# Performance work log

Measured on AMD Instinct MI355X. Metric: run time of the kernel, lower is better.

The kernel has to match this reference:

```python
import jax, jax.numpy as jnp
import numpy as np

B, T, V, E, H, D = 32, 64, 32000, 512, 1024, 1024
BOS, EOS, PAD, TAU = 1, 3, 0, 1.0


def setup_inputs() -> dict:
    key = jax.random.key(0)
    ks = jax.random.split(key, 8)
    s = lambda k, shape, sc=0.02: jax.random.normal(k, shape, jnp.float32) * sc
    return {
        'image_hidden': jax.random.normal(ks[0], (B, D), jnp.float32),
        'gumbel_u': jax.random.uniform(ks[1], (T, B, V), jnp.float32),
        'W_proj': s(ks[2], (H, D)), 'b_proj': jnp.zeros((H,), jnp.float32),
        'emb': s(ks[3], (V, E)),
        'W_ih': s(ks[4], (4 * H, E)), 'W_hh': s(ks[5], (4 * H, H)),
        'b_ih': jnp.zeros((4 * H,), jnp.float32), 'b_hh': jnp.zeros((4 * H,), jnp.float32),
        'W_hv': s(ks[6], (V, H)), 'b_hv': jnp.zeros((V,), jnp.float32),
    }


def lstm_cell(x, h, c, W_ih, W_hh, b_ih, b_hh):
    gates = x @ W_ih.T + h @ W_hh.T + (b_ih + b_hh)
    i, f, g, o = jnp.split(gates, 4, axis=-1)  # torch LSTM gate order
    c = jax.nn.sigmoid(f) * c + jax.nn.sigmoid(i) * jnp.tanh(g)
    h = jax.nn.sigmoid(o) * jnp.tanh(c)
    return h, c


def reference(image_hidden, gumbel_u, W_proj, b_proj, emb, W_ih, W_hh, b_ih, b_hh, W_hv, b_hv):
    # initial state from projected image representation
    h0 = image_hidden @ W_proj.T + b_proj            # [B, H]
    c0 = jnp.zeros_like(h0)
    x0 = jnp.broadcast_to(emb[BOS], (B, E))          # BOS embedding
    h, c = lstm_cell(x0, h0, c0, W_ih, W_hh, b_ih, b_hh)

    def step(carry, u):
        h, c = carry
        logit = h @ W_hv.T + b_hv                    # [B, V]
        g = -jnp.log(-jnp.log(u + 1e-10) + 1e-10)    # gumbel noise from uniform
        y_soft = jax.nn.softmax((logit + g) / TAU, axis=-1)
        label = jnp.argmax(y_soft, axis=-1)          # [B]
        y_hard = jax.nn.one_hot(label, V, dtype=y_soft.dtype)
        y = y_hard + y_soft - jax.lax.stop_gradient(y_soft)  # straight-through (hard=True)
        x = y @ emb                                  # soft embedding lookup [B, E]
        h, c = lstm_cell(x, h, c, W_ih, W_hh, b_ih, b_hh)
        return (h, c), (y, label)

    _, (ys, labels) = jax.lax.scan(step, (h, c), gumbel_u)
    logits = jnp.swapaxes(ys, 0, 1)                  # [B, T, V]
    labels = labels.T                                # [B, T]

    # force final token to EOS
    logits = logits.at[:, -1, :].set(jax.nn.one_hot(EOS, V, dtype=logits.dtype))
    labels = labels.at[:, -1].set(EOS)

    pad_g = jnp.cumsum((labels == EOS).astype(jnp.int32), axis=1) == 0  # True before first EOS
    message_ids = jnp.where(pad_g, labels, 0)
    pad_oh = jax.nn.one_hot(PAD, V, dtype=logits.dtype)
    message_logits = jnp.where(pad_g[:, :, None], logits, pad_oh)
    message_lengths = jnp.max(jnp.cumsum(pad_g.astype(jnp.int32), axis=1), axis=1) + 1
    return message_ids, message_logits, message_lengths
```

## Files before the change

kernel.cpp:

```cpp
#include <hip/hip_runtime.h>
#include <cstdint>
#include <cstddef>

#define NB 32
#define NT 64
#define NV 32000
#define NE 512
#define NH 1024
#define BOS_ID 1
#define EOS_ID 3

__device__ __forceinline__ unsigned mono_f32(float f) {
    unsigned u = __float_as_uint(f);
    return (u & 0x80000000u) ? ~u : (u | 0x80000000u);
}

__global__ __launch_bounds__(256) void k_init(const float* __restrict__ img,
                                              const float* __restrict__ Wp,
                                              const float* __restrict__ bp,
                                              float* __restrict__ h0,
                                              float* __restrict__ c) {
    int g = blockIdx.x * 256 + threadIdx.x;
    int j = g >> 5, b = g & 31;
    const float* ir = img + (size_t)b * NH;
    const float* wr = Wp + (size_t)j * NH;
    float s = bp[j];
    for (int k = 0; k < NH; k++) s = fmaf(ir[k], wr[k], s);
    h0[b * NH + j] = s;
    c[b * NH + j]  = 0.0f;
}

__global__ __launch_bounds__(256) void k_logit(const float* __restrict__ h,
                                               const float* __restrict__ Whv,
                                               const float* __restrict__ bhv,
                                               const float* __restrict__ gu,
                                               int s,
                                               unsigned long long* __restrict__ partials) {
    __shared__ float hs[32][36];
    __shared__ float wsh[32][132];
    __shared__ float red_s[32][32];
    __shared__ int   red_i[32][32];
    const int tid = threadIdx.x;
    const int blk = blockIdx.x;
    const int v0  = blk * 128;
    const int bq  = tid >> 5;
    const int vq  = tid & 31;
    float acc[4][4];
#pragma unroll
    for (int i = 0; i < 4; i++)
#pragma unroll
        for (int j = 0; j < 4; j++) acc[i][j] = 0.f;

    for (int kc = 0; kc < NH; kc += 32) {
        __syncthreads();
#pragma unroll
        for (int i = 0; i < 4; i++) {
            int idx = i * 256 + tid;
            int b = idx >> 5, kk = idx & 31;
            hs[kk][b] = h[b * NH + kc + kk];
        }
#pragma unroll
        for (int i = 0; i < 16; i++) {
            int idx = i * 256 + tid;
            int vv = idx >> 5, kk = idx & 31;
            wsh[kk][vv] = Whv[(size_t)(v0 + vv) * NH + kc + kk];
        }
        __syncthreads();
#pragma unroll
        for (int kk = 0; kk < 32; kk++) {
            float4 hv4 = *(const float4*)&hs[kk][bq * 4];
            float4 wv4 = *(const float4*)&wsh[kk][vq * 4];
            float hv[4] = {hv4.x, hv4.y, hv4.z, hv4.w};
            float wv[4] = {wv4.x, wv4.y, wv4.z, wv4.w};
#pragma unroll
            for (int bi = 0; bi < 4; bi++)
#pragma unroll
                for (int vi = 0; vi < 4; vi++)
                    acc[bi][vi] = fmaf(hv[bi], wv[vi], acc[bi][vi]);
        }
    }

    const float4 bv4 = *(const float4*)&bhv[v0 + vq * 4];
    float bvv[4] = {bv4.x, bv4.y, bv4.z, bv4.w};
#pragma unroll
    for (int bi = 0; bi < 4; bi++) {
        int b = bq * 4 + bi;
        const float4 uv4 = *(const float4*)&gu[((size_t)s * NB + b) * NV + v0 + vq * 4];
        float uvv[4] = {uv4.x, uv4.y, uv4.z, uv4.w};
        float best = -3.4e38f;
        int bidx = v0 + vq * 4;
#pragma unroll
        for (int vi = 0; vi < 4; vi++) {
            float g  = -logf(-logf(uvv[vi] + 1e-10f) + 1e-10f);
            float sc = acc[bi][vi] + bvv[vi] + g;
            if (sc > best) { best = sc; bidx = v0 + vq * 4 + vi; }
        }
        red_s[b][vq] = best;
        red_i[b][vq] = bidx;
    }
    __syncthreads();
    if (tid < 32) {
        int b = tid;
        float bs = red_s[b][0];
        int   bi = red_i[b][0];
        for (int q = 1; q < 32; q++) {
            float v = red_s[b][q];
            if (v > bs) { bs = v; bi = red_i[b][q]; }
        }
        unsigned long long key =
            ((unsigned long long)mono_f32(bs) << 32) | (unsigned)(~(unsigned)bi);
        partials[blk * 32 + b] = key;
    }
}

__global__ __launch_bounds__(256) void k_lstm(const float* __restrict__ h,
                                              float* __restrict__ hn,
                                              float* __restrict__ cbuf,
                                              const float* __restrict__ emb,
                                              const float* __restrict__ Wih,
                                              const float* __restrict__ Whh,
                                              const float* __restrict__ bih,
                                              const float* __restrict__ bhh,
                                              const unsigned long long* __restrict__ partials,
                                              int* __restrict__ hist,
                                              int s, int skip) {
    __shared__ float Wt[512][20];
    __shared__ float xh[32][517];
    __shared__ int labels[32];
    const int tid = threadIdx.x, blk = blockIdx.x;
    const int b8 = tid >> 3, ks = tid & 7;

    if (s < 0) {
        if (tid < 32) labels[tid] = BOS_ID;
    } else {
        unsigned long long best = 0ull;
        for (int p = ks; p < 250; p += 8) {
            unsigned long long k = partials[p * 32 + b8];
            if (k > best) best = k;
        }
#pragma unroll
        for (int m = 1; m < 8; m <<= 1) {
            unsigned long long o = (unsigned long long)__shfl_xor((long long)best, m, 64);
            if (o > best) best = o;
        }
        if (ks == 0) labels[b8] = (int)(~(unsigned)best);
    }
    __syncthreads();
    if (s >= 0 && blk == 0 && tid < 32) hist[s * 32 + tid] = labels[tid];
    if (skip) return;

    const int j0 = blk * 4;
    float acc[16];
#pragma unroll
    for (int r = 0; r < 16; r++) acc[r] = 0.f;

    for (int chunk = 0; chunk < 3; chunk++) {
        __syncthreads();
#pragma unroll
        for (int i = 0; i < 32; i++) {
            int idx = i * 256 + tid;
            int slot = idx >> 9, k = idx & 511;
            int gate = slot >> 2, jj = slot & 3;
            int row = gate * NH + j0 + jj;
            float w = (chunk == 0) ? Wih[(size_t)row * NE + k]
                                   : Whh[(size_t)row * NH + (chunk - 1) * 512 + k];
            Wt[k][slot] = w;
        }
#pragma unroll
        for (int i = 0; i < 64; i++) {
            int idx = i * 256 + tid;
            int b = idx >> 9, k = idx & 511;
            float xv = (chunk == 0) ? emb[(size_t)labels[b] * NE + k]
                                    : h[b * NH + (chunk - 1) * 512 + k];
            xh[b][k] = xv;
        }
        __syncthreads();
#pragma unroll 4
        for (int i = 0; i < 64; i++) {
            int k = ks + 8 * i;
            float xv = xh[b8][k];
            const float4 w0 = *(const float4*)&Wt[k][0];
            const float4 w1 = *(const float4*)&Wt[k][4];
            const float4 w2 = *(const float4*)&Wt[k][8];
            const float4 w3 = *(const float4*)&Wt[k][12];
            acc[0]  = fmaf(xv, w0.x, acc[0]);  acc[1]  = fmaf(xv, w0.y, acc[1]);
            acc[2]  = fmaf(xv, w0.z, acc[2]);  acc[3]  = fmaf(xv, w0.w, acc[3]);
            acc[4]  = fmaf(xv, w1.x, acc[4]);  acc[5]  = fmaf(xv, w1.y, acc[5]);
            acc[6]  = fmaf(xv, w1.z, acc[6]);  acc[7]  = fmaf(xv, w1.w, acc[7]);
            acc[8]  = fmaf(xv, w2.x, acc[8]);  acc[9]  = fmaf(xv, w2.y, acc[9]);
            acc[10] = fmaf(xv, w2.z, acc[10]); acc[11] = fmaf(xv, w2.w, acc[11]);
            acc[12] = fmaf(xv, w3.x, acc[12]); acc[13] = fmaf(xv, w3.y, acc[13]);
            acc[14] = fmaf(xv, w3.z, acc[14]); acc[15] = fmaf(xv, w3.w, acc[15]);
        }
    }
#pragma unroll
    for (int m = 1; m < 8; m <<= 1)
#pragma unroll
        for (int r = 0; r < 16; r++) acc[r] += __shfl_xor(acc[r], m, 64);

    if (ks == 0) {
        int b = b8;
#pragma unroll
        for (int jj = 0; jj < 4; jj++) {
            int j = j0 + jj;
            float gi = acc[0 + jj]  + bih[j]          + bhh[j];
            float gf = acc[4 + jj]  + bih[NH + j]     + bhh[NH + j];
            float gg = acc[8 + jj]  + bih[2 * NH + j] + bhh[2 * NH + j];
            float go = acc[12 + jj] + bih[3 * NH + j] + bhh[3 * NH + j];
            float si = 1.f / (1.f + expf(-gi));
            float sf = 1.f / (1.f + expf(-gf));
            float so = 1.f / (1.f + expf(-go));
            float cn = sf * cbuf[b * NH + j] + si * tanhf(gg);
            float hv = so * tanhf(cn);
            cbuf[b * NH + j] = cn;
            hn[b * NH + j]   = hv;
        }
    }
}

__global__ __launch_bounds__(64) void k_out(const int* __restrict__ hist,
                                            float* __restrict__ out) {
    int b = threadIdx.x;
    if (b >= 32) return;
    int te = 63;
    for (int t = 0; t < 63; t++)
        if (hist[t * 32 + b] == EOS_ID) { te = t; break; }
    for (int t = 0; t < 64; t++) {
        int lab = (t < 63) ? hist[t * 32 + b] : EOS_ID;
        int id = (t < te) ? lab : 0;
        out[b * 64 + t] = (float)id;
    }
    out[2048 + (size_t)NB * NT * NV + b] = (float)(te + 1);
}

__global__ __launch_bounds__(256) void k_scatter(float* __restrict__ out) {
    const int bt = blockIdx.x;
    float* row = out + 2048 + (size_t)bt * NV;
    const int id = (int)out[bt];
    float4 z = make_float4(0.f, 0.f, 0.f, 0.f);
    for (int i = threadIdx.x; i < NV / 4; i += 256) ((float4*)row)[i] = z;
    __syncthreads();
    if (threadIdx.x == 0) row[id] = 1.0f;
}

extern "C" void kernel_launch(void* const* d_in, const int* in_sizes, int n_in,
                              void* d_out, int out_size, void* d_ws, size_t ws_size,
                              hipStream_t stream) {
    const float* img = (const float*)d_in[0];
    const float* gu  = (const float*)d_in[1];
    const float* Wp  = (const float*)d_in[2];
    const float* bp  = (const float*)d_in[3];
    const float* emb = (const float*)d_in[4];
    const float* Wih = (const float*)d_in[5];
    const float* Whh = (const float*)d_in[6];
    const float* bih = (const float*)d_in[7];
    const float* bhh = (const float*)d_in[8];
    const float* Whv = (const float*)d_in[9];
    const float* bhv = (const float*)d_in[10];
    float* out = (float*)d_out;

    float* scratch = out + 2048;
    float* hA = scratch;
    float* hB = scratch + 32768;
    float* cb = scratch + 65536;
    unsigned long long* partials = (unsigned long long*)(scratch + 98304);
    int* hist = (int*)(scratch + 98304 + 16000);

    k_init<<<128, 256, 0, stream>>>(img, Wp, bp, hB, cb);
    k_lstm<<<256, 256, 0, stream>>>(hB, hA, cb, emb, Wih, Whh, bih, bhh,
                                    (const unsigned long long*)nullptr, hist, -1, 0);
    for (int s = 0; s < 63; s++) {
        const float* hc = (s & 1) ? hB : hA;
        float* hn       = (s & 1) ? hA : hB;
        k_logit<<<250, 256, 0, stream>>>(hc, Whv, bhv, gu, s, partials);
        k_lstm<<<256, 256, 0, stream>>>(hc, hn, cb, emb, Wih, Whh, bih, bhh,
                                        partials, hist, s, (s == 62) ? 1 : 0);
    }
    k_out<<<1, 64, 0, stream>>>(hist, out);
    k_scatter<<<2048, 256, 0, stream>>>(out);
}
```

Baseline: 12.64 ms.

## Double-buffer logit GEMM tiles and reduce argmax via wave shuffles plus atomicMax

The vocab-projection kernel now uses 512 threads with a 2x4 register tile and a 64-wide K chunk. Shared-memory tiles are double-buffered and the next chunk is prefetched into registers while the current one is computed. The per-block argmax runs as a wave-level shuffle reduction and combines across blocks with a 64-bit atomicMax into a ping-pong slot, so the LSTM kernel no longer scans 250 partials per row. The LSTM kernel zeros the next slot for the following step, which relies on stream ordering between kernels and adds atomic contention on 32 addresses.

After: 12.43 ms. About the same (-1.6%).

```diff
diff --git a/kernel.cpp b/kernel.cpp
--- a/kernel.cpp
+++ b/kernel.cpp
@@ -9,6 +9,7 @@
 #define NH 1024
 #define BOS_ID 1
 #define EOS_ID 3
+#define KC 64
 
 __device__ __forceinline__ unsigned mono_f32(float f) {
     unsigned u = __float_as_uint(f);
@@ -30,86 +31,110 @@
     c[b * NH + j]  = 0.0f;
 }
 
-__global__ __launch_bounds__(256) void k_logit(const float* __restrict__ h,
+__global__ __launch_bounds__(512) void k_logit(const float* __restrict__ h,
                                                const float* __restrict__ Whv,
                                                const float* __restrict__ bhv,
                                                const float* __restrict__ gu,
                                                int s,
-                                               unsigned long long* __restrict__ partials) {
-    __shared__ float hs[32][36];
-    __shared__ float wsh[32][132];
-    __shared__ float red_s[32][32];
-    __shared__ int   red_i[32][32];
+                                               unsigned long long* __restrict__ slot) {
+    __shared__ float wsh[2][KC][132];
+    __shared__ float hs[2][KC][34];
     const int tid = threadIdx.x;
-    const int blk = blockIdx.x;
-    const int v0  = blk * 128;
+    const int v0  = blockIdx.x * 128;
+    const int vq  = tid & 31;
     const int bq  = tid >> 5;
-    const int vq  = tid & 31;
-    float acc[4][4];
-#pragma unroll
-    for (int i = 0; i < 4; i++)
-#pragma unroll
-        for (int j = 0; j < 4; j++) acc[i][j] = 0.f;
-
-    for (int kc = 0; kc < NH; kc += 32) {
+    const int wq  = tid & 15;
+    const int wv  = tid >> 4;
+
+    float4 wr[4];
+    float4 hr;
+    float acc[2][4];
+#pragma unroll
+    for (int bi = 0; bi < 2; bi++)
+#pragma unroll
+        for (int j = 0; j < 4; j++) acc[bi][j] = 0.f;
+
+    auto load_chunk = [&](int kc) {
+#pragma unroll
+        for (int i = 0; i < 4; i++) {
+            int vv = i * 32 + wv;
+            wr[i] = *(const float4*)&Whv[(size_t)(v0 + vv) * NH + kc + wq * 4];
+        }
+        hr = *(const float4*)&h[wv * NH + kc + wq * 4];
+    };
+    auto store_chunk = [&](int p) {
+#pragma unroll
+        for (int i = 0; i < 4; i++) {
+            int vv = i * 32 + wv;
+            wsh[p][wq * 4 + 0][vv] = wr[i].x;
+            wsh[p][wq * 4 + 1][vv] = wr[i].y;
+            wsh[p][wq * 4 + 2][vv] = wr[i].z;
+            wsh[p][wq * 4 + 3][vv] = wr[i].w;
+        }
+        hs[p][wq * 4 + 0][wv] = hr.x;
+        hs[p][wq * 4 + 1][wv] = hr.y;
+        hs[p][wq * 4 + 2][wv] = hr.z;
+        hs[p][wq * 4 + 3][wv] = hr.w;
+    };
+
+    load_chunk(0);
+    store_chunk(0);
+    load_chunk(KC);
+
+    const int NCH = NH / KC;
+    for (int c = 0; c < NCH; c++) {
         __syncthreads();
-#pragma unroll
-        for (int i = 0; i < 4; i++) {
-            int idx = i * 256 + tid;
-            int b = idx >> 5, kk = idx & 31;
-            hs[kk][b] = h[b * NH + kc + kk];
-        }
-#pragma unroll
-        for (int i = 0; i < 16; i++) {
-            int idx = i * 256 + tid;
-            int vv = idx >> 5, kk = idx & 31;
-            wsh[kk][vv] = Whv[(size_t)(v0 + vv) * NH + kc + kk];
-        }
-        __syncthreads();
-#pragma unroll
-        for (int kk = 0; kk < 32; kk++) {
-            float4 hv4 = *(const float4*)&hs[kk][bq * 4];
-            float4 wv4 = *(const float4*)&wsh[kk][vq * 4];
-            float hv[4] = {hv4.x, hv4.y, hv4.z, hv4.w};
-            float wv[4] = {wv4.x, wv4.y, wv4.z, wv4.w};
-#pragma unroll
-            for (int bi = 0; bi < 4; bi++)
-#pragma unroll
-                for (int vi = 0; vi < 4; vi++)
-                    acc[bi][vi] = fmaf(hv[bi], wv[vi], acc[bi][vi]);
+        const int p = c & 1;
+#pragma unroll 16
+        for (int kk = 0; kk < KC; kk++) {
+            float4 wv4 = *(const float4*)&wsh[p][kk][vq * 4];
+            float2 hv2 = *(const float2*)&hs[p][kk][bq * 2];
+            acc[0][0] = fmaf(hv2.x, wv4.x, acc[0][0]);
+            acc[0][1] = fmaf(hv2.x, wv4.y, acc[0][1]);
+            acc[0][2] = fmaf(hv2.x, wv4.z, acc[0][2]);
+            acc[0][3] = fmaf(hv2.x, wv4.w, acc[0][3]);
+            acc[1][0] = fmaf(hv2.y, wv4.x, acc[1][0]);
+            acc[1][1] = fmaf(hv2.y, wv4.y, acc[1][1]);
+            acc[1][2] = fmaf(hv2.y, wv4.z, acc[1][2]);
+            acc[1][3] = fmaf(hv2.y, wv4.w, acc[1][3]);
+        }
+        if (c + 1 < NCH) {
+            store_chunk(1 - p);
+            if (c + 2 < NCH) load_chunk((c + 2) * KC);
         }
     }
 
     const float4 bv4 = *(const float4*)&bhv[v0 + vq * 4];
     float bvv[4] = {bv4.x, bv4.y, bv4.z, bv4.w};
-#pragma unroll
-    for (int bi = 0; bi < 4; bi++) {
-        int b = bq * 4 + bi;
-        const float4 uv4 = *(const float4*)&gu[((size_t)s * NB + b) * NV + v0 + vq * 4];
-        float uvv[4] = {uv4.x, uv4.y, uv4.z, uv4.w};
+    unsigned long long key[2];
+#pragma unroll
+    for (int bi = 0; bi < 2; bi++) {
+        int b = bq * 2 + bi;
+        const float4 u4 = *(const float4*)&gu[((size_t)s * NB + b) * NV + v0 + vq * 4];
+        float uvv[4] = {u4.x, u4.y, u4.z, u4.w};
         float best = -3.4e38f;
         int bidx = v0 + vq * 4;
 #pragma unroll
-        for (int vi = 0; vi < 4; vi++) {
-            float g  = -logf(-logf(uvv[vi] + 1e-10f) + 1e-10f);
-            float sc = acc[bi][vi] + bvv[vi] + g;
-            if (sc > best) { best = sc; bidx = v0 + vq * 4 + vi; }
-        }
-        red_s[b][vq] = best;
-        red_i[b][vq] = bidx;
-    }
-    __syncthreads();
-    if (tid < 32) {
-        int b = tid;
-        float bs = red_s[b][0];
-        int   bi = red_i[b][0];
-        for (int q = 1; q < 32; q++) {
-            float v = red_s[b][q];
-            if (v > bs) { bs = v; bi = red_i[b][q]; }
-        }
-        unsigned long long key =
-            ((unsigned long long)mono_f32(bs) << 32) | (unsigned)(~(unsigned)bi);
-        partials[blk * 32 + b] = key;
+        for (int j = 0; j < 4; j++) {
+            float g  = -logf(-logf(uvv[j] + 1e-10f) + 1e-10f);
+            float sc = acc[bi][j] + bvv[j] + g;
+            if (sc > best) { best = sc; bidx = v0 + vq * 4 + j; }
+        }
+        key[bi] = ((unsigned long long)mono_f32(best) << 32) | (unsigned)(~(unsigned)bidx);
+    }
+#pragma unroll
+    for (int m = 1; m < 32; m <<= 1) {
+#pragma unroll
+        for (int bi = 0; bi < 2; bi++) {
+            unsigned long long o =
+                (unsigned long long)__shfl_xor((long long)key[bi], m, 32);
+            if (o > key[bi]) key[bi] = o;
+        }
+    }
+    if (vq == 0) {
+#pragma unroll
+        for (int bi = 0; bi < 2; bi++)
+            atomicMax(&slot[(s & 1) * 32 + bq * 2 + bi], key[bi]);
     }
 }
 
@@ -121,7 +146,7 @@
                                               const float* __restrict__ Whh,
                                               const float* __restrict__ bih,
                                               const float* __restrict__ bhh,
-                                              const unsigned long long* __restrict__ partials,
+                                              unsigned long long* __restrict__ slot,
                                               int* __restrict__ hist,
                                               int s, int skip) {
     __shared__ float Wt[512][20];
@@ -133,19 +158,10 @@
     if (s < 0) {
         if (tid < 32) labels[tid] = BOS_ID;
     } else {
-        unsigned long long best = 0ull;
-        for (int p = ks; p < 250; p += 8) {
-            unsigned long long k = partials[p * 32 + b8];
-            if (k > best) best = k;
-        }
-#pragma unroll
-        for (int m = 1; m < 8; m <<= 1) {
-            unsigned long long o = (unsigned long long)__shfl_xor((long long)best, m, 64);
-            if (o > best) best = o;
-        }
-        if (ks == 0) labels[b8] = (int)(~(unsigned)best);
-    }
-    __syncthreads();
+        if (tid < 32) labels[tid] = (int)(~(unsigned)slot[(s & 1) * 32 + tid]);
+    }
+    if (tid >= 32 && tid < 64)
+        slot[((s + 1) & 1) * 32 + (tid - 32)] = 0ull;
     if (s >= 0 && blk == 0 && tid < 32) hist[s * 32 + tid] = labels[tid];
     if (skip) return;
 
@@ -159,12 +175,12 @@
 #pragma unroll
         for (int i = 0; i < 32; i++) {
             int idx = i * 256 + tid;
-            int slot = idx >> 9, k = idx & 511;
-            int gate = slot >> 2, jj = slot & 3;
+            int slot_i = idx >> 9, k = idx & 511;
+            int gate = slot_i >> 2, jj = slot_i & 3;
             int row = gate * NH + j0 + jj;
             float w = (chunk == 0) ? Wih[(size_t)row * NE + k]
                                    : Whh[(size_t)row * NH + (chunk - 1) * 512 + k];
-            Wt[k][slot] = w;
+            Wt[k][slot_i] = w;
         }
 #pragma unroll
         for (int i = 0; i < 64; i++) {
@@ -263,18 +279,18 @@
     float* hA = scratch;
     float* hB = scratch + 32768;
     float* cb = scratch + 65536;
-    unsigned long long* partials = (unsigned long long*)(scratch + 98304);
-    int* hist = (int*)(scratch + 98304 + 16000);
+    unsigned long long* slot = (unsigned long long*)(scratch + 98304);
+    int* hist = (int*)(scratch + 98304 + 128);
 
     k_init<<<128, 256, 0, stream>>>(img, Wp, bp, hB, cb);
     k_lstm<<<256, 256, 0, stream>>>(hB, hA, cb, emb, Wih, Whh, bih, bhh,
-                                    (const unsigned long long*)nullptr, hist, -1, 0);
+                                    slot, hist, -1, 0);
     for (int s = 0; s < 63; s++) {
         const float* hc = (s & 1) ? hB : hA;
         float* hn       = (s & 1) ? hA : hB;
-        k_logit<<<250, 256, 0, stream>>>(hc, Whv, bhv, gu, s, partials);
+        k_logit<<<250, 512, 0, stream>>>(hc, Whv, bhv, gu, s, slot);
         k_lstm<<<256, 256, 0, stream>>>(hc, hn, cb, emb, Wih, Whh, bih, bhh,
-                                        partials, hist, s, (s == 62) ? 1 : 0);
+                                        slot, hist, s, (s == 62) ? 1 : 0);
     }
     k_out<<<1, 64, 0, stream>>>(hist, out);
     k_scatter<<<2048, 256, 0, stream>>>(out);
```
